# Kernel tuning notes

Hardware: AMD Instinct MI355X
Metric: run time of the kernel (lower is better)

Reference implementation:

```python
import jax, jax.numpy as jnp
import numpy as np

EPS = 1e-10


def setup_inputs() -> dict:
    key = jax.random.key(0)
    k1, k2, k3, k4, k5, k6 = jax.random.split(key, 6)
    N, F_IN, F_OUT, R = 200000, 128, 128, 16
    B, S = 4096, 10  # batch of target nodes, sampled neighbors per node
    emb = jax.random.normal(k1, (N, F_IN), dtype=jnp.float32)
    w_self = jax.random.normal(k2, (F_OUT, F_IN), dtype=jnp.float32) * 0.05
    w_rel = jax.random.normal(k3, (R, F_OUT, F_IN), dtype=jnp.float32) * 0.05
    nodes = jax.random.randint(k4, (B,), 0, N, dtype=jnp.int32)
    neighbors = jax.random.randint(k5, (B, S), 0, N, dtype=jnp.int32)
    rel_mask = jax.random.randint(k6, (B, S, R), 0, 2, dtype=jnp.int32)
    return {"emb": emb, "w_self": w_self, "w_rel": w_rel,
            "nodes": nodes, "neighbors": neighbors, "rel_mask": rel_mask}


def reference(emb, w_self, w_rel, nodes, neighbors, rel_mask):
    # Self term: x @ W_self^T
    x = emb[nodes]                                   # [B, Fin]  (gather)
    out = x @ w_self.T                               # [B, Fout]
    # Gather sampled neighbor embeddings
    ne = emb[neighbors]                              # [B, S, Fin] (irregular gather)
    m = rel_mask.astype(emb.dtype)                   # [B, S, R] binary relation masks
    # Per-relation masked sum over sampled neighbors
    sums = jnp.einsum('bsr,bsf->rbf', m, ne)         # [R, B, Fin]
    counts = jnp.transpose(m.sum(axis=1))[..., None] # [R, B, 1] neighbors per (rel,node)
    agg = sums / (counts + EPS)                      # masked mean (matches mask/= n+1e-10)
    # Per-relation weight matmul, summed into output
    out = out + jnp.einsum('rbf,rof->bo', agg, w_rel)
    return jax.nn.relu(out)
```

## Files before the change

### kernel.cpp

```cpp
#include <hip/hip_runtime.h>
#include <hip/hip_bf16.h>


#define BT      16
#define LDA     2184
#define NTHR    512
#define K_STEPS 68
#define W2_UNITS (K_STEPS * 8)
#define W2_BYTES (W2_UNITS * 64 * 16)

typedef __attribute__((ext_vector_type(8))) short short8;
typedef __attribute__((ext_vector_type(4))) float f32x4;

__device__ __forceinline__ unsigned int pk2_rne(float lo, float hi) {
  unsigned int r;
  asm("v_cvt_pk_bf16_f32 %0, %1, %2" : "=v"(r) : "v"(lo), "v"(hi));
  return r;
}

__global__ __launch_bounds__(256)
void wprep(const float* __restrict__ w_self, const float* __restrict__ w_rel,
           uint4* __restrict__ w2)
{
  const int u  = blockIdx.x * 4 + (threadIdx.x >> 6);
  const int l  = threadIdx.x & 63;
  const int ln = l & 15, lj = l >> 4;
  const int ks = u >> 3, ot = u & 7;
  const int o  = ot * 16 + ln;
  const int k0 = ks * 32 + lj * 8;
  const float* src;
  if (k0 < 128) src = w_self + o * 128 + k0;
  else {
    const int r = (k0 - 128) >> 7, kc = (k0 - 128) & 127;
    src = w_rel + ((size_t)(r * 128 + o)) * 128 + kc;
  }
  const float4 a = *(const float4*)src;
  const float4 b = *(const float4*)(src + 4);
  uint4 v;
  v.x = pk2_rne(a.x, a.y); v.y = pk2_rne(a.z, a.w);
  v.z = pk2_rne(b.x, b.y); v.w = pk2_rne(b.z, b.w);
  w2[u * 64 + l] = v;
}

template<bool USE_W2>
__global__ __launch_bounds__(NTHR, 2)
void rgcn_fused(const float* __restrict__ emb,
                const float* __restrict__ w_self,
                const float* __restrict__ w_rel,
                const int*   __restrict__ nodes,
                const int*   __restrict__ neighbors,
                const int*   __restrict__ rel_mask,
                const uint4* __restrict__ w2,
                float*       __restrict__ out)
{
  __shared__ alignas(16) char smem[80128];
  unsigned short* A_t = (unsigned short*)smem;
  float (*mscale)[10][16] = (float (*)[10][16])(smem + 69888);

  const int t  = threadIdx.x;
  const int b0 = blockIdx.x * BT;
  const int l  = t & 63;
  const int w  = t >> 6;

  if (t < 256) {
    const int bi = t >> 4, r = t & 15;
    const int* mp = rel_mask + (size_t)(b0 + bi) * 160 + r;
    int mb[10]; int c = 0;
    #pragma unroll
    for (int s = 0; s < 10; ++s) { mb[s] = mp[s * 16]; c += mb[s]; }
    const float inv = 1.0f / ((float)c + 1e-10f);
    #pragma unroll
    for (int s = 0; s < 10; ++s) mscale[bi][s][r] = mb[s] ? inv : 0.0f;
  }
  __syncthreads();

  {
    const int bi = t >> 5;
    const int f0 = (t & 31) * 4;
    const int b  = b0 + bi;
    const int node = nodes[b];
    int nb[10];
    #pragma unroll
    for (int s = 0; s < 10; ++s) nb[s] = neighbors[b * 10 + s];
    float4 ne[10];
    #pragma unroll
    for (int s = 0; s < 10; ++s)
      ne[s] = *(const float4*)(emb + (size_t)nb[s] * 128 + f0);
    const float4 x4 = *(const float4*)(emb + (size_t)node * 128 + f0);
    char* arow = (char*)A_t + bi * (LDA * 2);
    uint2 sv; sv.x = pk2_rne(x4.x, x4.y); sv.y = pk2_rne(x4.z, x4.w);
    *(uint2*)(arow + f0 * 2) = sv;

    #pragma unroll
    for (int rc = 0; rc < 4; ++rc) {
      float acc[4][4];
      #pragma unroll
      for (int rr = 0; rr < 4; ++rr) { acc[rr][0]=0.f; acc[rr][1]=0.f; acc[rr][2]=0.f; acc[rr][3]=0.f; }
      #pragma unroll
      for (int s = 0; s < 10; ++s) {
        const float4 ms = *(const float4*)(&mscale[bi][s][rc * 4]);
        const float m[4] = {ms.x, ms.y, ms.z, ms.w};
        const float4 v = ne[s];
        #pragma unroll
        for (int rr = 0; rr < 4; ++rr) {
          acc[rr][0] += m[rr] * v.x;
          acc[rr][1] += m[rr] * v.y;
          acc[rr][2] += m[rr] * v.z;
          acc[rr][3] += m[rr] * v.w;
        }
      }
      #pragma unroll
      for (int rr = 0; rr < 4; ++rr) {
        const int r = rc * 4 + rr;
        uint2 v2; v2.x = pk2_rne(acc[rr][0], acc[rr][1]); v2.y = pk2_rne(acc[rr][2], acc[rr][3]);
        *(uint2*)(arow + 256 + r * 256 + f0 * 2) = v2;
      }
    }
  }
  __syncthreads();

  const int ln = l & 15, lj = l >> 4;
  f32x4 acc[8];
  #pragma unroll
  for (int ot = 0; ot < 8; ++ot) acc[ot] = (f32x4){0.f, 0.f, 0.f, 0.f};
  {
    const int ksb = (w < 4) ? w * 9 : 36 + (w - 4) * 8;
    const int kse = ksb + ((w < 4) ? 9 : 8);
    const char* arow = (const char*)A_t + ln * (LDA * 2);
    for (int ks = ksb; ks < kse; ++ks) {
      const short8 a = *(const short8*)(arow + ks * 64 + lj * 16);
      #pragma unroll
      for (int ot = 0; ot < 8; ++ot) {
        short8 bf;
        if constexpr (USE_W2) {
          union { uint4 u; short8 s; } wv;
          wv.u = w2[(ks * 8 + ot) * 64 + l];
          bf = wv.s;
        } else {
          const int o  = ot * 16 + ln;
          const int k0 = ks * 32 + lj * 8;
          const float* wp;
          if (k0 < 128) wp = w_self + o * 128 + k0;
          else {
            const int r = (k0 - 128) >> 7, kc = (k0 - 128) & 127;
            wp = w_rel + ((size_t)(r * 128 + o)) * 128 + kc;
          }
          const float4 wa = *(const float4*)wp;
          const float4 wb = *(const float4*)(wp + 4);
          union { unsigned int u[4]; short8 s; } cv;
          cv.u[0] = pk2_rne(wa.x, wa.y);
          cv.u[1] = pk2_rne(wa.z, wa.w);
          cv.u[2] = pk2_rne(wb.x, wb.y);
          cv.u[3] = pk2_rne(wb.z, wb.w);
          bf = cv.s;
        }
        acc[ot] = __builtin_amdgcn_mfma_f32_16x16x32_bf16(a, bf, acc[ot], 0, 0, 0);
      }
    }
  }
  __syncthreads();

  {
    float* P = (float*)smem;
    #pragma unroll
    for (int ot = 0; ot < 8; ++ot) {
      const int o = ot * 16 + ln;
      #pragma unroll
      for (int j = 0; j < 4; ++j)
        P[(w * 16 + lj * 4 + j) * 132 + o] = acc[ot][j];
    }
  }
  __syncthreads();

  {
    const float* P = (const float*)smem;
    const int row = t >> 5, o0 = (t & 31) * 4;
    f32x4 s = {0.f, 0.f, 0.f, 0.f};
    #pragma unroll
    for (int g = 0; g < 8; ++g)
      s += *(const f32x4*)(P + (g * 16 + row) * 132 + o0);
    float4 o4;
    o4.x = fmaxf(s[0], 0.f); o4.y = fmaxf(s[1], 0.f);
    o4.z = fmaxf(s[2], 0.f); o4.w = fmaxf(s[3], 0.f);
    *(float4*)(out + (size_t)(b0 + row) * 128 + o0) = o4;
  }
}

extern "C" void kernel_launch(void* const* d_in, const int* in_sizes, int n_in,
                              void* d_out, int out_size, void* d_ws, size_t ws_size,
                              hipStream_t stream) {
  const float* emb       = (const float*)d_in[0];
  const float* w_self    = (const float*)d_in[1];
  const float* w_rel     = (const float*)d_in[2];
  const int*   nodes     = (const int*)d_in[3];
  const int*   neighbors = (const int*)d_in[4];
  const int*   rel_mask  = (const int*)d_in[5];
  float* out = (float*)d_out;
  (void)in_sizes; (void)n_in; (void)out_size;

  if (d_ws != nullptr && ws_size >= (size_t)W2_BYTES) {
    wprep<<<136, 256, 0, stream>>>(w_self, w_rel, (uint4*)d_ws);
    rgcn_fused<true><<<4096 / BT, NTHR, 0, stream>>>(
        emb, w_self, w_rel, nodes, neighbors, rel_mask, (const uint4*)d_ws, out);
  } else {
    rgcn_fused<false><<<4096 / BT, NTHR, 0, stream>>>(
        emb, w_self, w_rel, nodes, neighbors, rel_mask, nullptr, out);
  }
}
```

Baseline: 25.75 us.

## Halve per-block node tile to 8 and remap threads for more blocks

Reduces the batch tile per block from 16 to 8 nodes, doubling the grid to 512 blocks and halving shared memory so four blocks can be resident per CU. Gather work is remapped so each wave handles one node with float2 loads and computes all 16 relation sums in one pass, and the mask loads are issued before the embedding gathers to overlap latency. The MFMA stage now runs with only 8 valid rows, so half of each 16-row MFMA tile is wasted and every block rereads the full bf16 weight buffer, doubling total weight traffic. The fallback path without a workspace is removed.

```diff
diff --git a/kernel.cpp b/kernel.cpp
--- a/kernel.cpp
+++ b/kernel.cpp
@@ -2,7 +2,7 @@
 #include <hip/hip_bf16.h>
 
 
-#define BT      16
+#define BT      8
 #define LDA     2184
 #define NTHR    512
 #define K_STEPS 68
@@ -42,80 +42,79 @@
   w2[u * 64 + l] = v;
 }
 
-template<bool USE_W2>
-__global__ __launch_bounds__(NTHR, 2)
+__global__ __launch_bounds__(NTHR, 4)
 void rgcn_fused(const float* __restrict__ emb,
-                const float* __restrict__ w_self,
-                const float* __restrict__ w_rel,
                 const int*   __restrict__ nodes,
                 const int*   __restrict__ neighbors,
                 const int*   __restrict__ rel_mask,
                 const uint4* __restrict__ w2,
                 float*       __restrict__ out)
 {
-  __shared__ alignas(16) char smem[80128];
+  __shared__ alignas(16) char smem[40064];
   unsigned short* A_t = (unsigned short*)smem;
-  float (*mscale)[10][16] = (float (*)[10][16])(smem + 69888);
+  float (*mscale)[10][16] = (float (*)[10][16])(smem + 34944);
 
   const int t  = threadIdx.x;
   const int b0 = blockIdx.x * BT;
   const int l  = t & 63;
   const int w  = t >> 6;
 
-  if (t < 256) {
-    const int bi = t >> 4, r = t & 15;
-    const int* mp = rel_mask + (size_t)(b0 + bi) * 160 + r;
-    int mb[10]; int c = 0;
+  int mb[10];
+  const int bi0 = t >> 4, r0 = t & 15;
+  if (t < 128) {
+    const int* mp = rel_mask + (size_t)(b0 + bi0) * 160 + r0;
     #pragma unroll
-    for (int s = 0; s < 10; ++s) { mb[s] = mp[s * 16]; c += mb[s]; }
+    for (int s = 0; s < 10; ++s) mb[s] = mp[s * 16];
+  }
+
+  const int bi = w;
+  const int f0 = l * 2;
+  const int b  = b0 + bi;
+  const int node = nodes[b];
+  int nb[10];
+  #pragma unroll
+  for (int s = 0; s < 10; ++s) nb[s] = neighbors[b * 10 + s];
+  float2 ne[10];
+  #pragma unroll
+  for (int s = 0; s < 10; ++s)
+    ne[s] = *(const float2*)(emb + (size_t)nb[s] * 128 + f0);
+  const float2 x2 = *(const float2*)(emb + (size_t)node * 128 + f0);
+
+  if (t < 128) {
+    int c = 0;
+    #pragma unroll
+    for (int s = 0; s < 10; ++s) c += mb[s];
     const float inv = 1.0f / ((float)c + 1e-10f);
     #pragma unroll
-    for (int s = 0; s < 10; ++s) mscale[bi][s][r] = mb[s] ? inv : 0.0f;
+    for (int s = 0; s < 10; ++s) mscale[bi0][s][r0] = mb[s] ? inv : 0.0f;
   }
   __syncthreads();
 
   {
-    const int bi = t >> 5;
-    const int f0 = (t & 31) * 4;
-    const int b  = b0 + bi;
-    const int node = nodes[b];
-    int nb[10];
+    char* arow = (char*)A_t + bi * (LDA * 2);
+    *(unsigned int*)(arow + f0 * 2) = pk2_rne(x2.x, x2.y);
+
+    float acc[16][2];
     #pragma unroll
-    for (int s = 0; s < 10; ++s) nb[s] = neighbors[b * 10 + s];
-    float4 ne[10];
+    for (int r = 0; r < 16; ++r) { acc[r][0] = 0.f; acc[r][1] = 0.f; }
     #pragma unroll
-    for (int s = 0; s < 10; ++s)
-      ne[s] = *(const float4*)(emb + (size_t)nb[s] * 128 + f0);
-    const float4 x4 = *(const float4*)(emb + (size_t)node * 128 + f0);
-    char* arow = (char*)A_t + bi * (LDA * 2);
-    uint2 sv; sv.x = pk2_rne(x4.x, x4.y); sv.y = pk2_rne(x4.z, x4.w);
-    *(uint2*)(arow + f0 * 2) = sv;
-
-    #pragma unroll
-    for (int rc = 0; rc < 4; ++rc) {
-      float acc[4][4];
+    for (int s = 0; s < 10; ++s) {
+      const float4 m0 = *(const float4*)(&mscale[bi][s][0]);
+      const float4 m1 = *(const float4*)(&mscale[bi][s][4]);
+      const float4 m2 = *(const float4*)(&mscale[bi][s][8]);
+      const float4 m3 = *(const float4*)(&mscale[bi][s][12]);
+      const float m[16] = {m0.x,m0.y,m0.z,m0.w, m1.x,m1.y,m1.z,m1.w,
+                           m2.x,m2.y,m2.z,m2.w, m3.x,m3.y,m3.z,m3.w};
+      const float2 v = ne[s];
       #pragma unroll
-      for (int rr = 0; rr < 4; ++rr) { acc[rr][0]=0.f; acc[rr][1]=0.f; acc[rr][2]=0.f; acc[rr][3]=0.f; }
-      #pragma unroll
-      for (int s = 0; s < 10; ++s) {
-        const float4 ms = *(const float4*)(&mscale[bi][s][rc * 4]);
-        const float m[4] = {ms.x, ms.y, ms.z, ms.w};
-        const float4 v = ne[s];
-        #pragma unroll
-        for (int rr = 0; rr < 4; ++rr) {
-          acc[rr][0] += m[rr] * v.x;
-          acc[rr][1] += m[rr] * v.y;
-          acc[rr][2] += m[rr] * v.z;
-          acc[rr][3] += m[rr] * v.w;
-        }
-      }
-      #pragma unroll
-      for (int rr = 0; rr < 4; ++rr) {
-        const int r = rc * 4 + rr;
-        uint2 v2; v2.x = pk2_rne(acc[rr][0], acc[rr][1]); v2.y = pk2_rne(acc[rr][2], acc[rr][3]);
-        *(uint2*)(arow + 256 + r * 256 + f0 * 2) = v2;
+      for (int r = 0; r < 16; ++r) {
+        acc[r][0] += m[r] * v.x;
+        acc[r][1] += m[r] * v.y;
       }
     }
+    #pragma unroll
+    for (int r = 0; r < 16; ++r)
+      *(unsigned int*)(arow + 256 + r * 256 + f0 * 2) = pk2_rne(acc[r][0], acc[r][1]);
   }
   __syncthreads();
 
@@ -126,35 +125,14 @@
   {
     const int ksb = (w < 4) ? w * 9 : 36 + (w - 4) * 8;
     const int kse = ksb + ((w < 4) ? 9 : 8);
-    const char* arow = (const char*)A_t + ln * (LDA * 2);
+    const char* arow = (const char*)A_t + (ln & 7) * (LDA * 2);
     for (int ks = ksb; ks < kse; ++ks) {
       const short8 a = *(const short8*)(arow + ks * 64 + lj * 16);
       #pragma unroll
       for (int ot = 0; ot < 8; ++ot) {
-        short8 bf;
-        if constexpr (USE_W2) {
-          union { uint4 u; short8 s; } wv;
-          wv.u = w2[(ks * 8 + ot) * 64 + l];
-          bf = wv.s;
-        } else {
-          const int o  = ot * 16 + ln;
-          const int k0 = ks * 32 + lj * 8;
-          const float* wp;
-          if (k0 < 128) wp = w_self + o * 128 + k0;
-          else {
-            const int r = (k0 - 128) >> 7, kc = (k0 - 128) & 127;
-            wp = w_rel + ((size_t)(r * 128 + o)) * 128 + kc;
-          }
-          const float4 wa = *(const float4*)wp;
-          const float4 wb = *(const float4*)(wp + 4);
-          union { unsigned int u[4]; short8 s; } cv;
-          cv.u[0] = pk2_rne(wa.x, wa.y);
-          cv.u[1] = pk2_rne(wa.z, wa.w);
-          cv.u[2] = pk2_rne(wb.x, wb.y);
-          cv.u[3] = pk2_rne(wb.z, wb.w);
-          bf = cv.s;
-        }
-        acc[ot] = __builtin_amdgcn_mfma_f32_16x16x32_bf16(a, bf, acc[ot], 0, 0, 0);
+        union { uint4 u; short8 s; } wv;
+        wv.u = w2[(ks * 8 + ot) * 64 + l];
+        acc[ot] = __builtin_amdgcn_mfma_f32_16x16x32_bf16(a, wv.s, acc[ot], 0, 0, 0);
       }
     }
   }
@@ -162,27 +140,30 @@
 
   {
     float* P = (float*)smem;
-    #pragma unroll
-    for (int ot = 0; ot < 8; ++ot) {
-      const int o = ot * 16 + ln;
+    if (lj < 2) {
       #pragma unroll
-      for (int j = 0; j < 4; ++j)
-        P[(w * 16 + lj * 4 + j) * 132 + o] = acc[ot][j];
+      for (int ot = 0; ot < 8; ++ot) {
+        const int o = ot * 16 + ln;
+        #pragma unroll
+        for (int j = 0; j < 4; ++j)
+          P[(w * 8 + lj * 4 + j) * 132 + o] = acc[ot][j];
+      }
     }
   }
   __syncthreads();
 
   {
     const float* P = (const float*)smem;
-    const int row = t >> 5, o0 = (t & 31) * 4;
-    f32x4 s = {0.f, 0.f, 0.f, 0.f};
+    const int row = w;
+    const int o0 = l * 2;
+    float s0 = 0.f, s1 = 0.f;
     #pragma unroll
-    for (int g = 0; g < 8; ++g)
-      s += *(const f32x4*)(P + (g * 16 + row) * 132 + o0);
-    float4 o4;
-    o4.x = fmaxf(s[0], 0.f); o4.y = fmaxf(s[1], 0.f);
-    o4.z = fmaxf(s[2], 0.f); o4.w = fmaxf(s[3], 0.f);
-    *(float4*)(out + (size_t)(b0 + row) * 128 + o0) = o4;
+    for (int g = 0; g < 8; ++g) {
+      const float2 p = *(const float2*)(P + (g * 8 + row) * 132 + o0);
+      s0 += p.x; s1 += p.y;
+    }
+    float2 o2; o2.x = fmaxf(s0, 0.f); o2.y = fmaxf(s1, 0.f);
+    *(float2*)(out + (size_t)(b0 + row) * 128 + o0) = o2;
   }
 }
 
@@ -196,14 +177,9 @@
   const int*   neighbors = (const int*)d_in[4];
   const int*   rel_mask  = (const int*)d_in[5];
   float* out = (float*)d_out;
-  (void)in_sizes; (void)n_in; (void)out_size;
+  (void)in_sizes; (void)n_in; (void)out_size; (void)ws_size;
 
-  if (d_ws != nullptr && ws_size >= (size_t)W2_BYTES) {
-    wprep<<<136, 256, 0, stream>>>(w_self, w_rel, (uint4*)d_ws);
-    rgcn_fused<true><<<4096 / BT, NTHR, 0, stream>>>(
-        emb, w_self, w_rel, nodes, neighbors, rel_mask, (const uint4*)d_ws, out);
-  } else {
-    rgcn_fused<false><<<4096 / BT, NTHR, 0, stream>>>(
-        emb, w_self, w_rel, nodes, neighbors, rel_mask, nullptr, out);
-  }
+  wprep<<<136, 256, 0, stream>>>(w_self, w_rel, (uint4*)d_ws);
+  rgcn_fused<<<4096 / BT, NTHR, 0, stream>>>(
+      emb, nodes, neighbors, rel_mask, (const uint4*)d_ws, out);
 }
```

New measurement: 26.78 us. 1.04x slower.
